# Performance work log

Measured on AMD Instinct MI355X. Metric: run time of the kernel, lower is better.

The kernel has to match this reference:

```python
import jax, jax.numpy as jnp
import numpy as np

N = 100000      # nodes
E = 3200000     # edges (before self loops)
IN, H, OUT = 512, 256, 64
K = 10
TEMP = 1.5
EPS = 1e-5


def setup_inputs() -> dict:
    key = jax.random.key(0)
    ks = jax.random.split(key, 16)
    def lin(k, fan_in, fan_out):
        lim = 1.0 / np.sqrt(fan_in)
        kw, kb = jax.random.split(k)
        w = jax.random.uniform(kw, (fan_in, fan_out), jnp.float32, -lim, lim)
        b = jax.random.uniform(kb, (fan_out,), jnp.float32, -lim, lim)
        return w, b
    w1, b1 = lin(ks[0], IN, H)
    w2, b2 = lin(ks[1], H, H)
    w3, b3 = lin(ks[2], H, H)
    w4, b4 = lin(ks[3], H, OUT)
    return {
        "x": jax.random.normal(ks[4], (N, IN), jnp.float32),
        "edge_index": jax.random.randint(ks[5], (2, E), 0, N, jnp.int64),
        "w1": w1, "b1": b1, "g1": jnp.ones((H,), jnp.float32), "be1": jnp.zeros((H,), jnp.float32),
        "w2": w2, "b2": b2, "g2": jnp.ones((H,), jnp.float32), "be2": jnp.zeros((H,), jnp.float32),
        "w3": w3, "b3": b3, "g3": jnp.ones((H,), jnp.float32), "be3": jnp.zeros((H,), jnp.float32),
        "w4": w4, "b4": b4,
        "alpha": jnp.full((K + 1,), 1.0 / (K + 1), jnp.float32),
    }


def _bn(h, g, b):
    # batch-statistics BatchNorm1d (training-mode normalization, biased var)
    m = h.mean(axis=0)
    v = ((h - m) ** 2).mean(axis=0)
    return g * (h - m) * jax.lax.rsqrt(v + EPS) + b


def reference(x, edge_index, w1, b1, g1, be1, w2, b2, g2, be2,
              w3, b3, g3, be3, w4, b4, alpha):
    n = x.shape[0]
    # add self loops
    loop = jnp.arange(n, dtype=edge_index.dtype)
    row = jnp.concatenate([edge_index[0], loop])
    col = jnp.concatenate([edge_index[1], loop])
    # symmetric normalization D^{-1/2} A D^{-1/2} (degree counted on row)
    deg = jax.ops.segment_sum(jnp.ones_like(row, x.dtype), row, num_segments=n)
    dinv = jnp.where(deg > 0, jax.lax.rsqrt(deg), 0.0)
    norm = dinv[row] * dinv[col]  # [E+N]

    gelu = lambda h: jax.nn.gelu(h, approximate=False)
    x0 = gelu(_bn(x @ w1 + b1, g1, be1))
    x1 = gelu(_bn(x0 @ w2 + b2, g2, be2) + x0)   # dropout=identity (eval)
    x2 = gelu(_bn(x1 @ w3 + b3, g3, be3) + x1)
    h = x2 @ w4 + b4                              # [N, OUT]

    def step(carry, a):
        xt, acc = carry
        xt = jax.ops.segment_sum(norm[:, None] * xt[col], row, num_segments=n)
        return (xt, acc + a * xt), None

    (_, acc), _ = jax.lax.scan(step, (h, alpha[0] * h), alpha[1:])
    return acc / TEMP
```

## Files before the change

kernel.cpp:

```cpp
#include <hip/hip_runtime.h>
#include <math.h>

#define N_NODES 100000
#define N_IN 512
#define N_H 256
#define N_OUT 64
#define KHOP 10
#define EPS_BN 1e-5f
#define INV_TEMP (1.0f/1.5f)

using half8  = __attribute__((ext_vector_type(8))) _Float16;
using half4  = __attribute__((ext_vector_type(4))) _Float16;
using floatx4 = __attribute__((ext_vector_type(4))) float;

struct ZPtrs { const _Float16* p[KHOP]; };


__global__ void init_kernel(int* __restrict__ deg, int* __restrict__ cursor, int n) {
    int i = blockIdx.x * blockDim.x + threadIdx.x;
    if (i < n) { deg[i] = 1; cursor[i] = 0; }
}

__global__ void count_kernel(const int* __restrict__ ei, int* __restrict__ deg, int E) {
    int i = blockIdx.x * blockDim.x + threadIdx.x;
    if (i < E) atomicAdd(&deg[ei[i]], 1);
}

__global__ void scan1_kernel(const int* __restrict__ deg, int* __restrict__ excl,
                             int* __restrict__ bsum, int n) {
    __shared__ int sd[256];
    int t = threadIdx.x;
    int base = blockIdx.x * 1024 + t * 4;
    int v0 = (base + 0 < n) ? deg[base + 0] : 0;
    int v1 = (base + 1 < n) ? deg[base + 1] : 0;
    int v2 = (base + 2 < n) ? deg[base + 2] : 0;
    int v3 = (base + 3 < n) ? deg[base + 3] : 0;
    int tot = v0 + v1 + v2 + v3;
    sd[t] = tot;
    __syncthreads();
    for (int off = 1; off < 256; off <<= 1) {
        int x = (t >= off) ? sd[t - off] : 0;
        __syncthreads();
        sd[t] += x;
        __syncthreads();
    }
    int run = sd[t] - tot;
    if (t == 255) bsum[blockIdx.x] = sd[t];
    if (base + 0 < n) excl[base + 0] = run; run += v0;
    if (base + 1 < n) excl[base + 1] = run; run += v1;
    if (base + 2 < n) excl[base + 2] = run; run += v2;
    if (base + 3 < n) excl[base + 3] = run;
}

__global__ void scan2_kernel(int* __restrict__ bsum, int nb) {
    __shared__ int sd[128];
    int t = threadIdx.x;
    int v = (t < nb) ? bsum[t] : 0;
    sd[t] = v;
    __syncthreads();
    for (int off = 1; off < 128; off <<= 1) {
        int x = (t >= off) ? sd[t - off] : 0;
        __syncthreads();
        sd[t] += x;
        __syncthreads();
    }
    if (t < nb) bsum[t] = sd[t] - v;
}

__global__ void scan3_kernel(int* __restrict__ row_ptr, const int* __restrict__ bsum,
                             const int* __restrict__ deg, float* __restrict__ dinv,
                             float* __restrict__ dinv2, float* __restrict__ sqd,
                             int n, int total) {
    int i = blockIdx.x * blockDim.x + threadIdx.x;
    if (i < n) {
        row_ptr[i] += bsum[i >> 10];
        float d = (float)deg[i];
        dinv[i]  = rsqrtf(d);
        dinv2[i] = 1.0f / d;
        sqd[i]   = sqrtf(d);
    }
    if (i == 0) row_ptr[n] = total;
}

__global__ void fill_kernel(const int* __restrict__ ei, int* __restrict__ cursor,
                            const int* __restrict__ row_ptr,
                            int* __restrict__ colv, int E, int n, int r0, int r1) {
    int i = blockIdx.x * blockDim.x + threadIdx.x;
    if (i >= E + n) return;
    int r, c;
    if (i < E) { r = ei[i]; c = ei[E + i]; }
    else       { r = i - E; c = r; }
    if (r < r0 || r >= r1) return;
    int pos = row_ptr[r] + atomicAdd(&cursor[r], 1);
    colv[pos] = c;
}


__global__ void cvt_f16_kernel(const float* __restrict__ in, _Float16* __restrict__ out,
                               int total4) {
    int i = blockIdx.x * blockDim.x + threadIdx.x;
    if (i >= total4) return;
    float4 v = reinterpret_cast<const float4*>(in)[i];
    half4 h;
    h.x = (_Float16)v.x; h.y = (_Float16)v.y; h.z = (_Float16)v.z; h.w = (_Float16)v.w;
    reinterpret_cast<half4*>(out)[i] = h;
}

__global__ void cvt_wT_kernel(const float* __restrict__ w, _Float16* __restrict__ wT,
                              int K, int N) {
    int i = blockIdx.x * blockDim.x + threadIdx.x;
    if (i >= K * N) return;
    int k = i / N, n = i - k * N;
    wT[(size_t)n * K + k] = (_Float16)w[i];
}


template<int KDIM, int NDIM, int BN, bool STATS, bool WRITE_Z, typename CT>
__global__ __launch_bounds__(256) void gemm_mfma_kernel(
    const _Float16* __restrict__ A, const _Float16* __restrict__ BT,
    const float* __restrict__ bias, CT* __restrict__ C, int M,
    float* __restrict__ sums, const float* __restrict__ dinv,
    _Float16* __restrict__ z0) {
    constexpr int BM = 128;
    constexpr int LDK = 40;
    constexpr int WTN = BN / 32;
    __shared__ _Float16 As[BM * LDK];
    __shared__ _Float16 Bs[BN * LDK];
    __shared__ float cs[BN];
    __shared__ float cq[BN];
    int t = threadIdx.x;
    int mbase = blockIdx.y * BM;
    int nbase = blockIdx.x * BN;
    int wv = t >> 6, lane = t & 63;
    int wm = (wv & 1) * 64;
    int wn = (wv >> 1) * (BN / 2);
    int q = lane >> 4;
    int fr = lane & 15;
    int sr = t >> 2;
    int sc = (t & 3) * 8;

    floatx4 acc[4][WTN];
    for (int mt = 0; mt < 4; ++mt)
        for (int nt = 0; nt < WTN; ++nt)
            acc[mt][nt] = floatx4{0.f, 0.f, 0.f, 0.f};

    for (int k0 = 0; k0 < KDIM; k0 += 32) {
        #pragma unroll
        for (int p = 0; p < 2; ++p) {
            int row = sr + p * 64;
            int grow = mbase + row;
            half8 v = {};
            if (grow < M)
                v = *reinterpret_cast<const half8*>(&A[(size_t)grow * KDIM + k0 + sc]);
            *reinterpret_cast<half8*>(&As[row * LDK + sc]) = v;
        }
        #pragma unroll
        for (int p = 0; p < BN / 64; ++p) {
            int row = sr + p * 64;
            half8 v = *reinterpret_cast<const half8*>(&BT[(size_t)(nbase + row) * KDIM + k0 + sc]);
            *reinterpret_cast<half8*>(&Bs[row * LDK + sc]) = v;
        }
        __syncthreads();
        half8 af[4], bf[WTN];
        #pragma unroll
        for (int mt = 0; mt < 4; ++mt)
            af[mt] = *reinterpret_cast<const half8*>(&As[(wm + mt * 16 + fr) * LDK + q * 8]);
        #pragma unroll
        for (int nt = 0; nt < WTN; ++nt)
            bf[nt] = *reinterpret_cast<const half8*>(&Bs[(wn + nt * 16 + fr) * LDK + q * 8]);
        #pragma unroll
        for (int mt = 0; mt < 4; ++mt)
            #pragma unroll
            for (int nt = 0; nt < WTN; ++nt)
                acc[mt][nt] = __builtin_amdgcn_mfma_f32_16x16x32_f16(af[mt], bf[nt], acc[mt][nt], 0, 0, 0);
        __syncthreads();
    }
    if constexpr (STATS) {
        if (t < BN) { cs[t] = 0.f; cq[t] = 0.f; }
        __syncthreads();
    }
    #pragma unroll
    for (int nt = 0; nt < WTN; ++nt) {
        int col = nbase + wn + nt * 16 + fr;
        float bv = bias[col];
        float s = 0.f, s2 = 0.f;
        #pragma unroll
        for (int mt = 0; mt < 4; ++mt) {
            #pragma unroll
            for (int rr = 0; rr < 4; ++rr) {
                int row = mbase + wm + mt * 16 + q * 4 + rr;
                if (row < M) {
                    float v = acc[mt][nt][rr] + bv;
                    C[(size_t)row * NDIM + col] = (CT)v;
                    if constexpr (STATS) { s += v; s2 += v * v; }
                    if constexpr (WRITE_Z)
                        z0[((size_t)row << 6) + col] = (_Float16)(dinv[row] * v);
                }
            }
        }
        if constexpr (STATS) {
            s  += __shfl_xor(s, 16);  s  += __shfl_xor(s, 32);
            s2 += __shfl_xor(s2, 16); s2 += __shfl_xor(s2, 32);
            if (q == 0) {
                atomicAdd(&cs[wn + nt * 16 + fr], s);
                atomicAdd(&cq[wn + nt * 16 + fr], s2);
            }
        }
    }
    if constexpr (STATS) {
        __syncthreads();
        if (t < BN) {
            atomicAdd(&sums[nbase + t], cs[t]);
            atomicAdd(&sums[N_H + nbase + t], cq[t]);
        }
    }
}


__global__ void finalize_stats_kernel(const float* __restrict__ sums,
                                      const float* __restrict__ g, const float* __restrict__ be,
                                      float* __restrict__ ab, float invM) {
    int c = threadIdx.x;
    float mean = sums[c] * invM;
    float var = sums[N_H + c] * invM - mean * mean;
    float a = g[c] * rsqrtf(var + EPS_BN);
    ab[c] = a;
    ab[N_H + c] = be[c] - mean * a;
}

__global__ void bn_gelu_kernel(const _Float16* __restrict__ T, const float* __restrict__ ab,
                               const _Float16* __restrict__ res, _Float16* __restrict__ Y,
                               int total4) {
    int i = blockIdx.x * blockDim.x + threadIdx.x;
    if (i >= total4) return;
    int c0 = (i * 4) & (N_H - 1);
    half4 tv = reinterpret_cast<const half4*>(T)[i];
    float4 av = *reinterpret_cast<const float4*>(&ab[c0]);
    float4 bv = *reinterpret_cast<const float4*>(&ab[N_H + c0]);
    float v0 = av.x * (float)tv.x + bv.x;
    float v1 = av.y * (float)tv.y + bv.y;
    float v2 = av.z * (float)tv.z + bv.z;
    float v3 = av.w * (float)tv.w + bv.w;
    if (res) {
        half4 rv = reinterpret_cast<const half4*>(res)[i];
        v0 += (float)rv.x; v1 += (float)rv.y; v2 += (float)rv.z; v3 += (float)rv.w;
    }
    half4 o;
    o.x = (_Float16)(0.5f * v0 * (1.f + erff(v0 * 0.70710678118654752f)));
    o.y = (_Float16)(0.5f * v1 * (1.f + erff(v1 * 0.70710678118654752f)));
    o.z = (_Float16)(0.5f * v2 * (1.f + erff(v2 * 0.70710678118654752f)));
    o.w = (_Float16)(0.5f * v3 * (1.f + erff(v3 * 0.70710678118654752f)));
    reinterpret_cast<half4*>(Y)[i] = o;
}


__global__ __launch_bounds__(256) void prop_kernel(
    const _Float16* __restrict__ zin, _Float16* __restrict__ zout,
    const int* __restrict__ colv, const int* __restrict__ row_ptr,
    const float* __restrict__ dinv2, int n) {
    int r = (blockIdx.x << 2) + (threadIdx.x >> 6);
    if (r >= n) return;
    int lane = threadIdx.x & 63;
    int esub = lane >> 4;
    int fo = (lane & 15) << 2;
    int s = __builtin_amdgcn_readfirstlane(row_ptr[r]);
    int e = __builtin_amdgcn_readfirstlane(row_ptr[r + 1]);
    float a0 = 0.f, a1 = 0.f, a2 = 0.f, a3 = 0.f;
    int i = s;
    for (; i + 16 <= e; i += 16) {
        int c0 = colv[i + esub];
        int c1 = colv[i + 4 + esub];
        int c2 = colv[i + 8 + esub];
        int c3 = colv[i + 12 + esub];
        half4 v0 = *reinterpret_cast<const half4*>(&zin[((size_t)c0 << 6) + fo]);
        half4 v1 = *reinterpret_cast<const half4*>(&zin[((size_t)c1 << 6) + fo]);
        half4 v2 = *reinterpret_cast<const half4*>(&zin[((size_t)c2 << 6) + fo]);
        half4 v3 = *reinterpret_cast<const half4*>(&zin[((size_t)c3 << 6) + fo]);
        a0 += (float)v0.x + (float)v1.x + (float)v2.x + (float)v3.x;
        a1 += (float)v0.y + (float)v1.y + (float)v2.y + (float)v3.y;
        a2 += (float)v0.z + (float)v1.z + (float)v2.z + (float)v3.z;
        a3 += (float)v0.w + (float)v1.w + (float)v2.w + (float)v3.w;
    }
    for (; i + 4 <= e; i += 4) {
        int c = colv[i + esub];
        half4 v = *reinterpret_cast<const half4*>(&zin[((size_t)c << 6) + fo]);
        a0 += (float)v.x; a1 += (float)v.y; a2 += (float)v.z; a3 += (float)v.w;
    }
    int rem = e - i;
    if (esub < rem) {
        int c = colv[i + esub];
        half4 v = *reinterpret_cast<const half4*>(&zin[((size_t)c << 6) + fo]);
        a0 += (float)v.x; a1 += (float)v.y; a2 += (float)v.z; a3 += (float)v.w;
    }
    a0 += __shfl_xor(a0, 16); a1 += __shfl_xor(a1, 16);
    a2 += __shfl_xor(a2, 16); a3 += __shfl_xor(a3, 16);
    a0 += __shfl_xor(a0, 32); a1 += __shfl_xor(a1, 32);
    a2 += __shfl_xor(a2, 32); a3 += __shfl_xor(a3, 32);
    if (lane < 16) {
        float d = dinv2[r];
        half4 o;
        o.x = (_Float16)(a0 * d); o.y = (_Float16)(a1 * d);
        o.z = (_Float16)(a2 * d); o.w = (_Float16)(a3 * d);
        *reinterpret_cast<half4*>(&zout[((size_t)r << 6) + fo]) = o;
    }
}

__global__ void prop_final_kernel(const float* __restrict__ h, ZPtrs zp,
                                  const float* __restrict__ sqd,
                                  const float* __restrict__ alpha,
                                  float* __restrict__ out, int total4) {
    int i = blockIdx.x * blockDim.x + threadIdx.x;
    if (i >= total4) return;
    int r = i >> 4;
    float4 hv = reinterpret_cast<const float4*>(h)[i];
    float s0 = 0.f, s1 = 0.f, s2 = 0.f, s3 = 0.f;
    #pragma unroll
    for (int k = 0; k < KHOP; ++k) {
        half4 z = reinterpret_cast<const half4*>(zp.p[k])[i];
        float ak = alpha[k + 1];
        s0 += ak * (float)z.x; s1 += ak * (float)z.y;
        s2 += ak * (float)z.z; s3 += ak * (float)z.w;
    }
    float sq = sqd[r];
    float a0 = alpha[0];
    float4 o;
    o.x = INV_TEMP * (a0 * hv.x + sq * s0);
    o.y = INV_TEMP * (a0 * hv.y + sq * s1);
    o.z = INV_TEMP * (a0 * hv.z + sq * s2);
    o.w = INV_TEMP * (a0 * hv.w + sq * s3);
    reinterpret_cast<float4*>(out)[i] = o;
}


extern "C" void kernel_launch(void* const* d_in, const int* in_sizes, int n_in,
                              void* d_out, int out_size, void* d_ws, size_t ws_size,
                              hipStream_t stream) {
    const float* x    = (const float*)d_in[0];
    const int*   ei   = (const int*)d_in[1];
    const float* w1   = (const float*)d_in[2];
    const float* b1   = (const float*)d_in[3];
    const float* g1   = (const float*)d_in[4];
    const float* be1  = (const float*)d_in[5];
    const float* w2   = (const float*)d_in[6];
    const float* b2   = (const float*)d_in[7];
    const float* g2   = (const float*)d_in[8];
    const float* be2  = (const float*)d_in[9];
    const float* w3   = (const float*)d_in[10];
    const float* b3   = (const float*)d_in[11];
    const float* g3   = (const float*)d_in[12];
    const float* be3  = (const float*)d_in[13];
    const float* w4   = (const float*)d_in[14];
    const float* b4   = (const float*)d_in[15];
    const float* alpha= (const float*)d_in[16];
    float* out = (float*)d_out;

    const int N = in_sizes[0] / N_IN;
    const int E = in_sizes[1] / 2;
    const int EN = E + N;
    const size_t NZ = (size_t)N * N_OUT;

    char* ws = (char*)d_ws;
    size_t off = 0;
    auto alloc = [&](size_t bytes) -> void* {
        void* p = ws + off;
        off = (off + bytes + 255) & ~(size_t)255;
        return p;
    };
    int*   deg     = (int*)alloc((size_t)N * 4);
    int*   cursor  = (int*)alloc((size_t)N * 4);
    int*   row_ptr = (int*)alloc((size_t)(N + 1) * 4);
    float* dinv    = (float*)alloc((size_t)N * 4);
    float* dinv2   = (float*)alloc((size_t)N * 4);
    float* sqd     = (float*)alloc((size_t)N * 4);
    int*   colv    = (int*)alloc((size_t)EN * 4);
    int*   bsum    = (int*)alloc(128 * 4);
    float* sums    = (float*)alloc(2 * N_H * 4);
    float* ab      = (float*)alloc(2 * N_H * 4);
    _Float16* w1T  = (_Float16*)alloc((size_t)N_IN * N_H * 2);
    _Float16* w2T  = (_Float16*)alloc((size_t)N_H * N_H * 2);
    _Float16* w3T  = (_Float16*)alloc((size_t)N_H * N_H * 2);
    _Float16* w4T  = (_Float16*)alloc((size_t)N_H * N_OUT * 2);
    _Float16* xh   = (_Float16*)alloc((size_t)N * N_IN * 2);
    float* T       = (float*)alloc((size_t)N * N_H * 4);
    _Float16* Ah0  = (_Float16*)alloc((size_t)N * N_H * 2);
    _Float16* Ah1  = (_Float16*)alloc((size_t)N * N_H * 2);
    float* hbuf    = (float*)alloc((size_t)N * N_OUT * 4);
    _Float16* z0   = (_Float16*)alloc(NZ * 2);

    _Float16* Tf16 = (_Float16*)T;

    _Float16* zk[KHOP + 1];
    zk[0] = z0;
    for (int k = 1; k <= 8; ++k) zk[k] = (_Float16*)T + (size_t)(k - 1) * NZ;
    zk[9]  = (_Float16*)Ah1;
    zk[10] = (_Float16*)Ah1 + NZ;

    const int TB = 256;
    int nbN  = (N + TB - 1) / TB;
    int nbE  = (E + TB - 1) / TB;
    int nbEN = (EN + TB - 1) / TB;
    int nscan = (N + 1023) / 1024;

    init_kernel<<<nbN, TB, 0, stream>>>(deg, cursor, N);
    count_kernel<<<nbE, TB, 0, stream>>>(ei, deg, E);
    scan1_kernel<<<nscan, TB, 0, stream>>>(deg, row_ptr, bsum, N);
    scan2_kernel<<<1, 128, 0, stream>>>(bsum, nscan);
    scan3_kernel<<<nbN, TB, 0, stream>>>(row_ptr, bsum, deg, dinv, dinv2, sqd, N, EN);
    {
        const int P = 4;
        int step = (N + P - 1) / P;
        for (int p = 0; p < P; ++p) {
            int r0 = p * step;
            int r1 = min(N, r0 + step);
            fill_kernel<<<nbEN, TB, 0, stream>>>(ei, cursor, row_ptr, colv, E, N, r0, r1);
        }
    }

    int x4 = N * N_IN / 4;
    cvt_f16_kernel<<<(x4 + TB - 1) / TB, TB, 0, stream>>>(x, xh, x4);
    cvt_wT_kernel<<<(N_IN * N_H + TB - 1) / TB, TB, 0, stream>>>(w1, w1T, N_IN, N_H);
    cvt_wT_kernel<<<(N_H * N_H + TB - 1) / TB, TB, 0, stream>>>(w2, w2T, N_H, N_H);
    cvt_wT_kernel<<<(N_H * N_H + TB - 1) / TB, TB, 0, stream>>>(w3, w3T, N_H, N_H);
    cvt_wT_kernel<<<(N_H * N_OUT + TB - 1) / TB, TB, 0, stream>>>(w4, w4T, N_H, N_OUT);

    int mt = (N + 127) / 128;
    int elemH4 = N * N_H / 4;
    int nbElemH4 = (elemH4 + TB - 1) / TB;

    hipMemsetAsync(sums, 0, 2 * N_H * 4, stream);
    gemm_mfma_kernel<N_IN, N_H, 128, true, false, _Float16><<<dim3(N_H / 128, mt), TB, 0, stream>>>(
        xh, w1T, b1, Tf16, N, sums, nullptr, nullptr);
    finalize_stats_kernel<<<1, N_H, 0, stream>>>(sums, g1, be1, ab, 1.0f / N);
    bn_gelu_kernel<<<nbElemH4, TB, 0, stream>>>(Tf16, ab, nullptr, Ah0, elemH4);
    hipMemsetAsync(sums, 0, 2 * N_H * 4, stream);
    gemm_mfma_kernel<N_H, N_H, 128, true, false, _Float16><<<dim3(N_H / 128, mt), TB, 0, stream>>>(
        Ah0, w2T, b2, Tf16, N, sums, nullptr, nullptr);
    finalize_stats_kernel<<<1, N_H, 0, stream>>>(sums, g2, be2, ab, 1.0f / N);
    bn_gelu_kernel<<<nbElemH4, TB, 0, stream>>>(Tf16, ab, Ah0, Ah1, elemH4);
    hipMemsetAsync(sums, 0, 2 * N_H * 4, stream);
    gemm_mfma_kernel<N_H, N_H, 128, true, false, _Float16><<<dim3(N_H / 128, mt), TB, 0, stream>>>(
        Ah1, w3T, b3, Tf16, N, sums, nullptr, nullptr);
    finalize_stats_kernel<<<1, N_H, 0, stream>>>(sums, g3, be3, ab, 1.0f / N);
    bn_gelu_kernel<<<nbElemH4, TB, 0, stream>>>(Tf16, ab, Ah1, Ah0, elemH4);
    gemm_mfma_kernel<N_H, N_OUT, 64, false, true, float><<<dim3(1, mt), TB, 0, stream>>>(
        Ah0, w4T, b4, hbuf, N, nullptr, dinv, z0);

    int nbProp = (N + 3) / 4;
    for (int k = 1; k <= KHOP; ++k) {
        prop_kernel<<<nbProp, TB, 0, stream>>>(zk[k - 1], zk[k], colv, row_ptr, dinv2, N);
    }

    ZPtrs zp;
    for (int k = 0; k < KHOP; ++k) zp.p[k] = zk[k + 1];
    int total4 = N * N_OUT / 4;
    prop_final_kernel<<<(total4 + TB - 1) / TB, TB, 0, stream>>>(hbuf, zp, sqd, alpha, out, total4);
}
```

Before: 1.648 ms.

## Record edge slot during degree count and fuse preprocessing conversions into one launch

The degree-count atomics now also return each edge's slot within its row, stored as a 16-bit value. The fill pass can then write colv without a second round of atomics. Self loops are placed by scan3 at the end of each row, and the x and weight fp16 conversions are merged with the count into one multi-role kernel, removing several launches. The risks are the extra pos array traffic and a 16-bit position that would overflow for nodes with degree above 65535, which random inputs with average degree 32 will not reach.

```diff
diff --git a/kernel.cpp b/kernel.cpp
--- a/kernel.cpp
+++ b/kernel.cpp
@@ -16,25 +16,78 @@
 struct ZPtrs { const _Float16* p[KHOP]; };
 
 
-__global__ void init_kernel(int* __restrict__ deg, int* __restrict__ cursor, int n) {
+__global__ void init_kernel(int* __restrict__ cnt, int n) {
     int i = blockIdx.x * blockDim.x + threadIdx.x;
-    if (i < n) { deg[i] = 1; cursor[i] = 0; }
-}
-
-__global__ void count_kernel(const int* __restrict__ ei, int* __restrict__ deg, int E) {
-    int i = blockIdx.x * blockDim.x + threadIdx.x;
-    if (i < E) atomicAdd(&deg[ei[i]], 1);
-}
-
-__global__ void scan1_kernel(const int* __restrict__ deg, int* __restrict__ excl,
+    if (i < n) cnt[i] = 0;
+}
+
+__global__ __launch_bounds__(256) void fused_pre_kernel(
+    const int* __restrict__ ei, int* __restrict__ cnt, unsigned short* __restrict__ pos,
+    const float* __restrict__ x, _Float16* __restrict__ xh,
+    const float* __restrict__ w1, _Float16* __restrict__ w1T,
+    const float* __restrict__ w2, _Float16* __restrict__ w2T,
+    const float* __restrict__ w3, _Float16* __restrict__ w3T,
+    const float* __restrict__ w4, _Float16* __restrict__ w4T,
+    int E, int nbE, int x4, int nbX4) {
+    int bid = blockIdx.x;
+    int t = threadIdx.x;
+    if (bid < nbE) {
+        int i = bid * 256 + t;
+        if (i < E) {
+            int r = ei[i];
+            pos[i] = (unsigned short)atomicAdd(&cnt[r], 1);
+        }
+        return;
+    }
+    bid -= nbE;
+    if (bid < nbX4) {
+        int i = bid * 256 + t;
+        if (i < x4) {
+            float4 v = reinterpret_cast<const float4*>(x)[i];
+            half4 h;
+            h.x = (_Float16)v.x; h.y = (_Float16)v.y; h.z = (_Float16)v.z; h.w = (_Float16)v.w;
+            reinterpret_cast<half4*>(xh)[i] = h;
+        }
+        return;
+    }
+    bid -= nbX4;
+    if (bid < 512) {
+        int i = bid * 256 + t;
+        int k = i >> 8, n = i & 255;
+        w1T[(size_t)n * 512 + k] = (_Float16)w1[i];
+        return;
+    }
+    bid -= 512;
+    if (bid < 256) {
+        int i = bid * 256 + t;
+        int k = i >> 8, n = i & 255;
+        w2T[(size_t)n * 256 + k] = (_Float16)w2[i];
+        return;
+    }
+    bid -= 256;
+    if (bid < 256) {
+        int i = bid * 256 + t;
+        int k = i >> 8, n = i & 255;
+        w3T[(size_t)n * 256 + k] = (_Float16)w3[i];
+        return;
+    }
+    bid -= 256;
+    {
+        int i = bid * 256 + t;
+        int k = i >> 6, n = i & 63;
+        w4T[(size_t)n * 256 + k] = (_Float16)w4[i];
+    }
+}
+
+__global__ void scan1_kernel(const int* __restrict__ cnt, int* __restrict__ excl,
                              int* __restrict__ bsum, int n) {
     __shared__ int sd[256];
     int t = threadIdx.x;
     int base = blockIdx.x * 1024 + t * 4;
-    int v0 = (base + 0 < n) ? deg[base + 0] : 0;
-    int v1 = (base + 1 < n) ? deg[base + 1] : 0;
-    int v2 = (base + 2 < n) ? deg[base + 2] : 0;
-    int v3 = (base + 3 < n) ? deg[base + 3] : 0;
+    int v0 = (base + 0 < n) ? cnt[base + 0] + 1 : 0;
+    int v1 = (base + 1 < n) ? cnt[base + 1] + 1 : 0;
+    int v2 = (base + 2 < n) ? cnt[base + 2] + 1 : 0;
+    int v3 = (base + 3 < n) ? cnt[base + 3] + 1 : 0;
     int tot = v0 + v1 + v2 + v3;
     sd[t] = tot;
     __syncthreads();
@@ -68,50 +121,31 @@
 }
 
 __global__ void scan3_kernel(int* __restrict__ row_ptr, const int* __restrict__ bsum,
-                             const int* __restrict__ deg, float* __restrict__ dinv,
+                             const int* __restrict__ cnt, float* __restrict__ dinv,
                              float* __restrict__ dinv2, float* __restrict__ sqd,
-                             int n, int total) {
+                             int* __restrict__ colv, int n, int total) {
     int i = blockIdx.x * blockDim.x + threadIdx.x;
     if (i < n) {
-        row_ptr[i] += bsum[i >> 10];
-        float d = (float)deg[i];
+        int rp = row_ptr[i] + bsum[i >> 10];
+        row_ptr[i] = rp;
+        int cv = cnt[i];
+        float d = (float)(cv + 1);
         dinv[i]  = rsqrtf(d);
         dinv2[i] = 1.0f / d;
         sqd[i]   = sqrtf(d);
+        colv[rp + cv] = i;
     }
     if (i == 0) row_ptr[n] = total;
 }
 
-__global__ void fill_kernel(const int* __restrict__ ei, int* __restrict__ cursor,
+__global__ void fill_kernel(const int* __restrict__ ei, const unsigned short* __restrict__ pos,
                             const int* __restrict__ row_ptr,
-                            int* __restrict__ colv, int E, int n, int r0, int r1) {
+                            int* __restrict__ colv, int E, int r0, int r1) {
     int i = blockIdx.x * blockDim.x + threadIdx.x;
-    if (i >= E + n) return;
-    int r, c;
-    if (i < E) { r = ei[i]; c = ei[E + i]; }
-    else       { r = i - E; c = r; }
+    if (i >= E) return;
+    int r = ei[i];
     if (r < r0 || r >= r1) return;
-    int pos = row_ptr[r] + atomicAdd(&cursor[r], 1);
-    colv[pos] = c;
-}
-
-
-__global__ void cvt_f16_kernel(const float* __restrict__ in, _Float16* __restrict__ out,
-                               int total4) {
-    int i = blockIdx.x * blockDim.x + threadIdx.x;
-    if (i >= total4) return;
-    float4 v = reinterpret_cast<const float4*>(in)[i];
-    half4 h;
-    h.x = (_Float16)v.x; h.y = (_Float16)v.y; h.z = (_Float16)v.z; h.w = (_Float16)v.w;
-    reinterpret_cast<half4*>(out)[i] = h;
-}
-
-__global__ void cvt_wT_kernel(const float* __restrict__ w, _Float16* __restrict__ wT,
-                              int K, int N) {
-    int i = blockIdx.x * blockDim.x + threadIdx.x;
-    if (i >= K * N) return;
-    int k = i / N, n = i - k * N;
-    wT[(size_t)n * K + k] = (_Float16)w[i];
+    colv[row_ptr[r] + pos[i]] = ei[E + i];
 }
 
 
@@ -366,13 +400,13 @@
         off = (off + bytes + 255) & ~(size_t)255;
         return p;
     };
-    int*   deg     = (int*)alloc((size_t)N * 4);
-    int*   cursor  = (int*)alloc((size_t)N * 4);
+    int*   cnt     = (int*)alloc((size_t)N * 4);
     int*   row_ptr = (int*)alloc((size_t)(N + 1) * 4);
     float* dinv    = (float*)alloc((size_t)N * 4);
     float* dinv2   = (float*)alloc((size_t)N * 4);
     float* sqd     = (float*)alloc((size_t)N * 4);
     int*   colv    = (int*)alloc((size_t)EN * 4);
+    unsigned short* pos = (unsigned short*)alloc((size_t)E * 2);
     int*   bsum    = (int*)alloc(128 * 4);
     float* sums    = (float*)alloc(2 * N_H * 4);
     float* ab      = (float*)alloc(2 * N_H * 4);
@@ -398,30 +432,31 @@
     const int TB = 256;
     int nbN  = (N + TB - 1) / TB;
     int nbE  = (E + TB - 1) / TB;
-    int nbEN = (EN + TB - 1) / TB;
     int nscan = (N + 1023) / 1024;
-
-    init_kernel<<<nbN, TB, 0, stream>>>(deg, cursor, N);
-    count_kernel<<<nbE, TB, 0, stream>>>(ei, deg, E);
-    scan1_kernel<<<nscan, TB, 0, stream>>>(deg, row_ptr, bsum, N);
+    int x4 = N * N_IN / 4;
+    int nbX4 = (x4 + TB - 1) / TB;
+
+    init_kernel<<<nbN, TB, 0, stream>>>(cnt, N);
+    {
+        int grid = nbE + nbX4 + 512 + 256 + 256 + 64;
+        fused_pre_kernel<<<grid, TB, 0, stream>>>(ei, cnt, pos, x, xh,
+                                                  w1, w1T, w2, w2T, w3, w3T, w4, w4T,
+                                                  E, nbE, x4, nbX4);
+    }
+
+    scan1_kernel<<<nscan, TB, 0, stream>>>(cnt, row_ptr, bsum, N);
     scan2_kernel<<<1, 128, 0, stream>>>(bsum, nscan);
-    scan3_kernel<<<nbN, TB, 0, stream>>>(row_ptr, bsum, deg, dinv, dinv2, sqd, N, EN);
+    scan3_kernel<<<nbN, TB, 0, stream>>>(row_ptr, bsum, cnt, dinv, dinv2, sqd, colv, N, EN);
+
     {
         const int P = 4;
         int step = (N + P - 1) / P;
         for (int p = 0; p < P; ++p) {
             int r0 = p * step;
             int r1 = min(N, r0 + step);
-            fill_kernel<<<nbEN, TB, 0, stream>>>(ei, cursor, row_ptr, colv, E, N, r0, r1);
-        }
-    }
-
-    int x4 = N * N_IN / 4;
-    cvt_f16_kernel<<<(x4 + TB - 1) / TB, TB, 0, stream>>>(x, xh, x4);
-    cvt_wT_kernel<<<(N_IN * N_H + TB - 1) / TB, TB, 0, stream>>>(w1, w1T, N_IN, N_H);
-    cvt_wT_kernel<<<(N_H * N_H + TB - 1) / TB, TB, 0, stream>>>(w2, w2T, N_H, N_H);
-    cvt_wT_kernel<<<(N_H * N_H + TB - 1) / TB, TB, 0, stream>>>(w3, w3T, N_H, N_H);
-    cvt_wT_kernel<<<(N_H * N_OUT + TB - 1) / TB, TB, 0, stream>>>(w4, w4T, N_H, N_OUT);
+            fill_kernel<<<nbE, TB, 0, stream>>>(ei, pos, row_ptr, colv, E, r0, r1);
+        }
+    }
 
     int mt = (N + 127) / 128;
     int elemH4 = N * N_H / 4;
```

New measurement: 1.522 ms. 1.08x faster.
